# Performance work log

Hardware: AMD Instinct MI355X
Metric: run time of the kernel (lower is better)

## Reference

```python
import jax, jax.numpy as jnp
import numpy as np

L1_W = 0.5
L2_W = 0.5
THR_W = 0.5
NON_THR_W = 0.5


def setup_inputs() -> dict:
    key = jax.random.key(0)
    k1, k2 = jax.random.split(key)
    shape = (32, 3, 512, 512)
    input_img = jax.random.normal(k1, shape, dtype=jnp.float32)
    target_img = jax.random.normal(k2, shape, dtype=jnp.float32)
    return {"input_img": input_img, "target_img": target_img}


def _masked_mean(x, mask):
    # mean over elements where mask is True; 0.0 if mask is empty
    cnt = jnp.sum(mask)
    s = jnp.sum(jnp.where(mask, x, 0.0))
    return jnp.where(cnt > 0, s / jnp.maximum(cnt, 1).astype(x.dtype), jnp.zeros((), x.dtype))


def reference(input_img, target_img):
    diff = input_img - target_img
    pixel_diff = jnp.abs(diff)          # |x - y|
    pixel_diff_sq = diff * diff          # (x - y)^2

    mse_loss = jnp.mean(pixel_diff_sq)
    mae_loss = jnp.mean(pixel_diff)

    # adaptive thresholds (mse_threshold / mae_threshold were None)
    mse_thresholded_loss = _masked_mean(pixel_diff_sq, pixel_diff_sq >= mse_loss)
    mae_thresholded_loss = _masked_mean(pixel_diff, pixel_diff >= mae_loss)

    combined_thr = L1_W * mae_thresholded_loss + L2_W * mse_thresholded_loss
    combined_non_thr = L1_W * mae_loss + L2_W * mse_loss

    total_loss = THR_W * combined_thr + NON_THR_W * combined_non_thr
    return total_loss
```

## Files before the change

kernel.cpp:

```cpp
#include <hip/hip_runtime.h>


#define THREADS 256
#define NB 2048
#define UNROLL 4

__device__ __forceinline__ float wave_reduce_f(float v) {
    for (int o = 32; o > 0; o >>= 1) v += __shfl_down(v, o);
    return v;
}
__device__ __forceinline__ unsigned wave_reduce_u(unsigned v) {
    for (int o = 32; o > 0; o >>= 1) v += __shfl_down(v, o);
    return v;
}
__device__ __forceinline__ double wave_reduce_d(double v) {
    for (int o = 32; o > 0; o >>= 1) v += __shfl_down(v, o);
    return v;
}

__global__ void pass1_sums(const float4* __restrict__ a, const float4* __restrict__ b,
                           int n4, int n, float* __restrict__ psq, float* __restrict__ pab) {
    float ssq = 0.f, sab = 0.f;
    const int tile_total = gridDim.x * blockDim.x * UNROLL;
    const int n4_main = (n4 / tile_total) * tile_total;

    for (int base = (blockIdx.x * blockDim.x) * UNROLL + threadIdx.x;
         base < n4_main; base += tile_total) {
        float4 xa[UNROLL], xb[UNROLL];
#pragma unroll
        for (int j = 0; j < UNROLL; ++j) {
            xa[j] = a[base + j * THREADS];
            xb[j] = b[base + j * THREADS];
        }
#pragma unroll
        for (int j = 0; j < UNROLL; ++j) {
            float d0 = xa[j].x - xb[j].x, d1 = xa[j].y - xb[j].y;
            float d2 = xa[j].z - xb[j].z, d3 = xa[j].w - xb[j].w;
            ssq += d0 * d0 + d1 * d1 + d2 * d2 + d3 * d3;
            sab += fabsf(d0) + fabsf(d1) + fabsf(d2) + fabsf(d3);
        }
    }
    for (int i = n4_main + blockIdx.x * blockDim.x + threadIdx.x; i < n4;
         i += gridDim.x * blockDim.x) {
        float4 x = a[i], y = b[i];
        float d0 = x.x - y.x, d1 = x.y - y.y, d2 = x.z - y.z, d3 = x.w - y.w;
        ssq += d0 * d0 + d1 * d1 + d2 * d2 + d3 * d3;
        sab += fabsf(d0) + fabsf(d1) + fabsf(d2) + fabsf(d3);
    }
    const float* as = (const float*)a;
    const float* bs = (const float*)b;
    for (int i = n4 * 4 + blockIdx.x * blockDim.x + threadIdx.x; i < n;
         i += gridDim.x * blockDim.x) {
        float d = as[i] - bs[i];
        ssq += d * d;
        sab += fabsf(d);
    }

    ssq = wave_reduce_f(ssq);
    sab = wave_reduce_f(sab);
    __shared__ float s1[THREADS / 64], s2[THREADS / 64];
    int lane = threadIdx.x & 63, wave = threadIdx.x >> 6;
    if (lane == 0) { s1[wave] = ssq; s2[wave] = sab; }
    __syncthreads();
    if (threadIdx.x == 0) {
        float t1 = 0.f, t2 = 0.f;
        for (int w = 0; w < THREADS / 64; ++w) { t1 += s1[w]; t2 += s2[w]; }
        psq[blockIdx.x] = t1;
        pab[blockIdx.x] = t2;
    }
}

__global__ void finalize_means(const float* __restrict__ psq, const float* __restrict__ pab,
                               float* __restrict__ means, int nb, double inv_n) {
    double s1 = 0.0, s2 = 0.0;
    for (int i = threadIdx.x; i < nb; i += blockDim.x) { s1 += psq[i]; s2 += pab[i]; }
    s1 = wave_reduce_d(s1);
    s2 = wave_reduce_d(s2);
    __shared__ double w1[THREADS / 64], w2[THREADS / 64];
    int lane = threadIdx.x & 63, wave = threadIdx.x >> 6;
    if (lane == 0) { w1[wave] = s1; w2[wave] = s2; }
    __syncthreads();
    if (threadIdx.x == 0) {
        double t1 = 0.0, t2 = 0.0;
        for (int w = 0; w < THREADS / 64; ++w) { t1 += w1[w]; t2 += w2[w]; }
        means[0] = (float)(t1 * inv_n);
        means[1] = (float)(t2 * inv_n);
    }
}

__global__ void pass2_masked(const float4* __restrict__ a, const float4* __restrict__ b,
                             int n4, int n, const float* __restrict__ means,
                             float* __restrict__ p2sq, float* __restrict__ p2ab,
                             unsigned* __restrict__ p2c1, unsigned* __restrict__ p2c2) {
    const float mse = means[0];
    const float mae = means[1];
    float mssq = 0.f, msab = 0.f;
    unsigned c1 = 0, c2 = 0;
    const int tile_total = gridDim.x * blockDim.x * UNROLL;
    const int n4_main = (n4 / tile_total) * tile_total;

    for (int base = (blockIdx.x * blockDim.x) * UNROLL + threadIdx.x;
         base < n4_main; base += tile_total) {
        float4 xa[UNROLL], xb[UNROLL];
#pragma unroll
        for (int j = 0; j < UNROLL; ++j) {
            xa[j] = a[base + j * THREADS];
            xb[j] = b[base + j * THREADS];
        }
#pragma unroll
        for (int j = 0; j < UNROLL; ++j) {
            float d[4] = {xa[j].x - xb[j].x, xa[j].y - xb[j].y,
                          xa[j].z - xb[j].z, xa[j].w - xb[j].w};
#pragma unroll
            for (int k = 0; k < 4; ++k) {
                float dsq = d[k] * d[k];
                float ad = fabsf(d[k]);
                if (dsq >= mse) { mssq += dsq; c1++; }
                if (ad >= mae)  { msab += ad;  c2++; }
            }
        }
    }
    for (int i = n4_main + blockIdx.x * blockDim.x + threadIdx.x; i < n4;
         i += gridDim.x * blockDim.x) {
        float4 x = a[i], y = b[i];
        float d[4] = {x.x - y.x, x.y - y.y, x.z - y.z, x.w - y.w};
#pragma unroll
        for (int k = 0; k < 4; ++k) {
            float dsq = d[k] * d[k];
            float ad = fabsf(d[k]);
            if (dsq >= mse) { mssq += dsq; c1++; }
            if (ad >= mae)  { msab += ad;  c2++; }
        }
    }
    const float* as = (const float*)a;
    const float* bs = (const float*)b;
    for (int i = n4 * 4 + blockIdx.x * blockDim.x + threadIdx.x; i < n;
         i += gridDim.x * blockDim.x) {
        float d = as[i] - bs[i];
        float dsq = d * d;
        float ad = fabsf(d);
        if (dsq >= mse) { mssq += dsq; c1++; }
        if (ad >= mae)  { msab += ad;  c2++; }
    }

    mssq = wave_reduce_f(mssq);
    msab = wave_reduce_f(msab);
    c1 = wave_reduce_u(c1);
    c2 = wave_reduce_u(c2);
    __shared__ float s1[THREADS / 64], s2[THREADS / 64];
    __shared__ unsigned u1[THREADS / 64], u2[THREADS / 64];
    int lane = threadIdx.x & 63, wave = threadIdx.x >> 6;
    if (lane == 0) { s1[wave] = mssq; s2[wave] = msab; u1[wave] = c1; u2[wave] = c2; }
    __syncthreads();
    if (threadIdx.x == 0) {
        float t1 = 0.f, t2 = 0.f;
        unsigned k1 = 0, k2 = 0;
        for (int w = 0; w < THREADS / 64; ++w) { t1 += s1[w]; t2 += s2[w]; k1 += u1[w]; k2 += u2[w]; }
        p2sq[blockIdx.x] = t1;
        p2ab[blockIdx.x] = t2;
        p2c1[blockIdx.x] = k1;
        p2c2[blockIdx.x] = k2;
    }
}

__global__ void finalize_loss(const float* __restrict__ p2sq, const float* __restrict__ p2ab,
                              const unsigned* __restrict__ p2c1, const unsigned* __restrict__ p2c2,
                              const float* __restrict__ means, int nb, float* __restrict__ out) {
    double s1 = 0.0, s2 = 0.0;
    unsigned long long k1 = 0, k2 = 0;
    for (int i = threadIdx.x; i < nb; i += blockDim.x) {
        s1 += p2sq[i]; s2 += p2ab[i]; k1 += p2c1[i]; k2 += p2c2[i];
    }
    s1 = wave_reduce_d(s1);
    s2 = wave_reduce_d(s2);
    for (int o = 32; o > 0; o >>= 1) k1 += __shfl_down(k1, o);
    for (int o = 32; o > 0; o >>= 1) k2 += __shfl_down(k2, o);
    __shared__ double w1[THREADS / 64], w2[THREADS / 64];
    __shared__ unsigned long long v1[THREADS / 64], v2[THREADS / 64];
    int lane = threadIdx.x & 63, wave = threadIdx.x >> 6;
    if (lane == 0) { w1[wave] = s1; w2[wave] = s2; v1[wave] = k1; v2[wave] = k2; }
    __syncthreads();
    if (threadIdx.x == 0) {
        double t1 = 0.0, t2 = 0.0;
        unsigned long long c1 = 0, c2 = 0;
        for (int w = 0; w < THREADS / 64; ++w) { t1 += w1[w]; t2 += w2[w]; c1 += v1[w]; c2 += v2[w]; }
        double mse_thr = c1 ? t1 / (double)c1 : 0.0;
        double mae_thr = c2 ? t2 / (double)c2 : 0.0;
        double comb_thr = 0.5 * mae_thr + 0.5 * mse_thr;
        double comb_non = 0.5 * (double)means[1] + 0.5 * (double)means[0];
        out[0] = (float)(0.5 * comb_thr + 0.5 * comb_non);
    }
}

extern "C" void kernel_launch(void* const* d_in, const int* in_sizes, int n_in,
                              void* d_out, int out_size, void* d_ws, size_t ws_size,
                              hipStream_t stream) {
    const float* a = (const float*)d_in[0];
    const float* b = (const float*)d_in[1];
    const int n = in_sizes[0];
    const int n4 = n / 4;

    char* ws = (char*)d_ws;
    float* p1sq = (float*)(ws + 0);
    float* p1ab = (float*)(ws + 8192);
    float* p2sq = (float*)(ws + 16384);
    float* p2ab = (float*)(ws + 24576);
    unsigned* p2c1 = (unsigned*)(ws + 32768);
    unsigned* p2c2 = (unsigned*)(ws + 40960);
    float* means = (float*)(ws + 49152);

    pass1_sums<<<NB, THREADS, 0, stream>>>((const float4*)a, (const float4*)b, n4, n, p1sq, p1ab);
    finalize_means<<<1, THREADS, 0, stream>>>(p1sq, p1ab, means, NB, 1.0 / (double)n);
    pass2_masked<<<NB, THREADS, 0, stream>>>((const float4*)a, (const float4*)b, n4, n, means,
                                             p2sq, p2ab, p2c1, p2c2);
    finalize_loss<<<1, THREADS, 0, stream>>>(p2sq, p2ab, p2c1, p2c2, means, NB, (float*)d_out);
}
```

Baseline: 250.9 us.

## Fuse mean finalization into pass2 and specialize exact-size fully unrolled passes

Removes the separate finalize_means launch: every pass2 block re-reduces the 2048 pass1 partials itself to get the thresholds, and the final kernel recomputes the means. Adds a specialized path for the exact input size (32*3*512*512) where each thread handles 12 float4s with fixed indexing, batched loads, no tail loops, and branchless masked accumulation. The aim is to save one kernel launch and gap, and to get more memory-level parallelism per thread. In exchange, each pass2 block redundantly reads 16KB of partials, and the general fallback path is kept for other sizes.

```diff
diff --git a/kernel.cpp b/kernel.cpp
--- a/kernel.cpp
+++ b/kernel.cpp
@@ -3,7 +3,8 @@
 
 #define THREADS 256
 #define NB 2048
-#define UNROLL 4
+#define PER_THREAD 12
+#define BATCH 6
 
 __device__ __forceinline__ float wave_reduce_f(float v) {
     for (int o = 32; o > 0; o >>= 1) v += __shfl_down(v, o);
@@ -18,129 +19,112 @@
     return v;
 }
 
-__global__ void pass1_sums(const float4* __restrict__ a, const float4* __restrict__ b,
-                           int n4, int n, float* __restrict__ psq, float* __restrict__ pab) {
-    float ssq = 0.f, sab = 0.f;
-    const int tile_total = gridDim.x * blockDim.x * UNROLL;
-    const int n4_main = (n4 / tile_total) * tile_total;
-
-    for (int base = (blockIdx.x * blockDim.x) * UNROLL + threadIdx.x;
-         base < n4_main; base += tile_total) {
-        float4 xa[UNROLL], xb[UNROLL];
-#pragma unroll
-        for (int j = 0; j < UNROLL; ++j) {
-            xa[j] = a[base + j * THREADS];
-            xb[j] = b[base + j * THREADS];
-        }
-#pragma unroll
-        for (int j = 0; j < UNROLL; ++j) {
-            float d0 = xa[j].x - xb[j].x, d1 = xa[j].y - xb[j].y;
-            float d2 = xa[j].z - xb[j].z, d3 = xa[j].w - xb[j].w;
-            ssq += d0 * d0 + d1 * d1 + d2 * d2 + d3 * d3;
-            sab += fabsf(d0) + fabsf(d1) + fabsf(d2) + fabsf(d3);
-        }
-    }
-    for (int i = n4_main + blockIdx.x * blockDim.x + threadIdx.x; i < n4;
-         i += gridDim.x * blockDim.x) {
-        float4 x = a[i], y = b[i];
-        float d0 = x.x - y.x, d1 = x.y - y.y, d2 = x.z - y.z, d3 = x.w - y.w;
-        ssq += d0 * d0 + d1 * d1 + d2 * d2 + d3 * d3;
-        sab += fabsf(d0) + fabsf(d1) + fabsf(d2) + fabsf(d3);
-    }
-    const float* as = (const float*)a;
-    const float* bs = (const float*)b;
-    for (int i = n4 * 4 + blockIdx.x * blockDim.x + threadIdx.x; i < n;
-         i += gridDim.x * blockDim.x) {
-        float d = as[i] - bs[i];
-        ssq += d * d;
-        sab += fabsf(d);
-    }
-
-    ssq = wave_reduce_f(ssq);
-    sab = wave_reduce_f(sab);
+__device__ __forceinline__ void block_reduce_2f(float& v1, float& v2, float* out1, float* out2) {
+    v1 = wave_reduce_f(v1);
+    v2 = wave_reduce_f(v2);
     __shared__ float s1[THREADS / 64], s2[THREADS / 64];
     int lane = threadIdx.x & 63, wave = threadIdx.x >> 6;
-    if (lane == 0) { s1[wave] = ssq; s2[wave] = sab; }
+    if (lane == 0) { s1[wave] = v1; s2[wave] = v2; }
     __syncthreads();
     if (threadIdx.x == 0) {
         float t1 = 0.f, t2 = 0.f;
         for (int w = 0; w < THREADS / 64; ++w) { t1 += s1[w]; t2 += s2[w]; }
-        psq[blockIdx.x] = t1;
-        pab[blockIdx.x] = t2;
-    }
-}
-
-__global__ void finalize_means(const float* __restrict__ psq, const float* __restrict__ pab,
-                               float* __restrict__ means, int nb, double inv_n) {
+        out1[blockIdx.x] = t1;
+        out2[blockIdx.x] = t2;
+    }
+}
+
+__device__ __forceinline__ void compute_means(const float* __restrict__ p1sq,
+                                              const float* __restrict__ p1ab,
+                                              double inv_n, float& mse, float& mae) {
     double s1 = 0.0, s2 = 0.0;
-    for (int i = threadIdx.x; i < nb; i += blockDim.x) { s1 += psq[i]; s2 += pab[i]; }
+    for (int i = threadIdx.x; i < NB; i += THREADS) { s1 += p1sq[i]; s2 += p1ab[i]; }
     s1 = wave_reduce_d(s1);
     s2 = wave_reduce_d(s2);
     __shared__ double w1[THREADS / 64], w2[THREADS / 64];
+    __shared__ float bm[2];
     int lane = threadIdx.x & 63, wave = threadIdx.x >> 6;
     if (lane == 0) { w1[wave] = s1; w2[wave] = s2; }
     __syncthreads();
     if (threadIdx.x == 0) {
         double t1 = 0.0, t2 = 0.0;
         for (int w = 0; w < THREADS / 64; ++w) { t1 += w1[w]; t2 += w2[w]; }
-        means[0] = (float)(t1 * inv_n);
-        means[1] = (float)(t2 * inv_n);
-    }
-}
-
-__global__ void pass2_masked(const float4* __restrict__ a, const float4* __restrict__ b,
-                             int n4, int n, const float* __restrict__ means,
-                             float* __restrict__ p2sq, float* __restrict__ p2ab,
-                             unsigned* __restrict__ p2c1, unsigned* __restrict__ p2c2) {
-    const float mse = means[0];
-    const float mae = means[1];
+        bm[0] = (float)(t1 * inv_n);
+        bm[1] = (float)(t2 * inv_n);
+    }
+    __syncthreads();
+    mse = bm[0];
+    mae = bm[1];
+    __syncthreads();
+}
+
+
+__global__ __launch_bounds__(THREADS) void pass1_s(const float4* __restrict__ a,
+                                                   const float4* __restrict__ b,
+                                                   float* __restrict__ psq,
+                                                   float* __restrict__ pab) {
+    const int i0 = blockIdx.x * (THREADS * PER_THREAD) + threadIdx.x;
+    float s0 = 0.f, s1 = 0.f, a0 = 0.f, a1 = 0.f;
+#pragma unroll
+    for (int h = 0; h < PER_THREAD / BATCH; ++h) {
+        const int base = i0 + h * BATCH * THREADS;
+        float4 xa[BATCH], xb[BATCH];
+#pragma unroll
+        for (int j = 0; j < BATCH; ++j) xa[j] = a[base + j * THREADS];
+#pragma unroll
+        for (int j = 0; j < BATCH; ++j) xb[j] = b[base + j * THREADS];
+#pragma unroll
+        for (int j = 0; j < BATCH; ++j) {
+            float d0 = xa[j].x - xb[j].x, d1 = xa[j].y - xb[j].y;
+            float d2 = xa[j].z - xb[j].z, d3 = xa[j].w - xb[j].w;
+            s0 += d0 * d0 + d1 * d1;
+            s1 += d2 * d2 + d3 * d3;
+            a0 += fabsf(d0) + fabsf(d1);
+            a1 += fabsf(d2) + fabsf(d3);
+        }
+    }
+    float ssq = s0 + s1, sab = a0 + a1;
+    block_reduce_2f(ssq, sab, psq, pab);
+}
+
+__global__ __launch_bounds__(THREADS) void pass2_s(const float4* __restrict__ a,
+                                                   const float4* __restrict__ b,
+                                                   const float* __restrict__ p1sq,
+                                                   const float* __restrict__ p1ab,
+                                                   double inv_n,
+                                                   float* __restrict__ p2sq,
+                                                   float* __restrict__ p2ab,
+                                                   unsigned* __restrict__ p2c1,
+                                                   unsigned* __restrict__ p2c2) {
+    float mse, mae;
+    compute_means(p1sq, p1ab, inv_n, mse, mae);
+
+    const int i0 = blockIdx.x * (THREADS * PER_THREAD) + threadIdx.x;
     float mssq = 0.f, msab = 0.f;
     unsigned c1 = 0, c2 = 0;
-    const int tile_total = gridDim.x * blockDim.x * UNROLL;
-    const int n4_main = (n4 / tile_total) * tile_total;
-
-    for (int base = (blockIdx.x * blockDim.x) * UNROLL + threadIdx.x;
-         base < n4_main; base += tile_total) {
-        float4 xa[UNROLL], xb[UNROLL];
-#pragma unroll
-        for (int j = 0; j < UNROLL; ++j) {
-            xa[j] = a[base + j * THREADS];
-            xb[j] = b[base + j * THREADS];
-        }
-#pragma unroll
-        for (int j = 0; j < UNROLL; ++j) {
+#pragma unroll
+    for (int h = 0; h < PER_THREAD / BATCH; ++h) {
+        const int base = i0 + h * BATCH * THREADS;
+        float4 xa[BATCH], xb[BATCH];
+#pragma unroll
+        for (int j = 0; j < BATCH; ++j) xa[j] = a[base + j * THREADS];
+#pragma unroll
+        for (int j = 0; j < BATCH; ++j) xb[j] = b[base + j * THREADS];
+#pragma unroll
+        for (int j = 0; j < BATCH; ++j) {
             float d[4] = {xa[j].x - xb[j].x, xa[j].y - xb[j].y,
                           xa[j].z - xb[j].z, xa[j].w - xb[j].w};
 #pragma unroll
             for (int k = 0; k < 4; ++k) {
                 float dsq = d[k] * d[k];
                 float ad = fabsf(d[k]);
-                if (dsq >= mse) { mssq += dsq; c1++; }
-                if (ad >= mae)  { msab += ad;  c2++; }
+                bool m1 = dsq >= mse, m2 = ad >= mae;
+                mssq += m1 ? dsq : 0.f;
+                msab += m2 ? ad : 0.f;
+                c1 += m1 ? 1u : 0u;
+                c2 += m2 ? 1u : 0u;
             }
         }
-    }
-    for (int i = n4_main + blockIdx.x * blockDim.x + threadIdx.x; i < n4;
-         i += gridDim.x * blockDim.x) {
-        float4 x = a[i], y = b[i];
-        float d[4] = {x.x - y.x, x.y - y.y, x.z - y.z, x.w - y.w};
-#pragma unroll
-        for (int k = 0; k < 4; ++k) {
-            float dsq = d[k] * d[k];
-            float ad = fabsf(d[k]);
-            if (dsq >= mse) { mssq += dsq; c1++; }
-            if (ad >= mae)  { msab += ad;  c2++; }
-        }
-    }
-    const float* as = (const float*)a;
-    const float* bs = (const float*)b;
-    for (int i = n4 * 4 + blockIdx.x * blockDim.x + threadIdx.x; i < n;
-         i += gridDim.x * blockDim.x) {
-        float d = as[i] - bs[i];
-        float dsq = d * d;
-        float ad = fabsf(d);
-        if (dsq >= mse) { mssq += dsq; c1++; }
-        if (ad >= mae)  { msab += ad;  c2++; }
     }
 
     mssq = wave_reduce_f(mssq);
@@ -163,32 +147,110 @@
     }
 }
 
-__global__ void finalize_loss(const float* __restrict__ p2sq, const float* __restrict__ p2ab,
-                              const unsigned* __restrict__ p2c1, const unsigned* __restrict__ p2c2,
-                              const float* __restrict__ means, int nb, float* __restrict__ out) {
-    double s1 = 0.0, s2 = 0.0;
+__global__ void finalize_loss_s(const float* __restrict__ p1sq, const float* __restrict__ p1ab,
+                                const float* __restrict__ p2sq, const float* __restrict__ p2ab,
+                                const unsigned* __restrict__ p2c1, const unsigned* __restrict__ p2c2,
+                                double inv_n, float* __restrict__ out) {
+    double s1 = 0.0, s2 = 0.0, m1 = 0.0, m2 = 0.0;
     unsigned long long k1 = 0, k2 = 0;
-    for (int i = threadIdx.x; i < nb; i += blockDim.x) {
-        s1 += p2sq[i]; s2 += p2ab[i]; k1 += p2c1[i]; k2 += p2c2[i];
-    }
-    s1 = wave_reduce_d(s1);
-    s2 = wave_reduce_d(s2);
+    for (int i = threadIdx.x; i < NB; i += blockDim.x) {
+        m1 += p1sq[i]; m2 += p1ab[i];
+        s1 += p2sq[i]; s2 += p2ab[i];
+        k1 += p2c1[i]; k2 += p2c2[i];
+    }
+    s1 = wave_reduce_d(s1); s2 = wave_reduce_d(s2);
+    m1 = wave_reduce_d(m1); m2 = wave_reduce_d(m2);
     for (int o = 32; o > 0; o >>= 1) k1 += __shfl_down(k1, o);
     for (int o = 32; o > 0; o >>= 1) k2 += __shfl_down(k2, o);
-    __shared__ double w1[THREADS / 64], w2[THREADS / 64];
+    __shared__ double w1[THREADS / 64], w2[THREADS / 64], w3[THREADS / 64], w4[THREADS / 64];
     __shared__ unsigned long long v1[THREADS / 64], v2[THREADS / 64];
     int lane = threadIdx.x & 63, wave = threadIdx.x >> 6;
-    if (lane == 0) { w1[wave] = s1; w2[wave] = s2; v1[wave] = k1; v2[wave] = k2; }
-    __syncthreads();
-    if (threadIdx.x == 0) {
-        double t1 = 0.0, t2 = 0.0;
+    if (lane == 0) { w1[wave] = s1; w2[wave] = s2; w3[wave] = m1; w4[wave] = m2; v1[wave] = k1; v2[wave] = k2; }
+    __syncthreads();
+    if (threadIdx.x == 0) {
+        double t1 = 0.0, t2 = 0.0, q1 = 0.0, q2 = 0.0;
         unsigned long long c1 = 0, c2 = 0;
-        for (int w = 0; w < THREADS / 64; ++w) { t1 += w1[w]; t2 += w2[w]; c1 += v1[w]; c2 += v2[w]; }
+        for (int w = 0; w < THREADS / 64; ++w) {
+            t1 += w1[w]; t2 += w2[w]; q1 += w3[w]; q2 += w4[w]; c1 += v1[w]; c2 += v2[w];
+        }
+        float mse = (float)(q1 * inv_n);
+        float mae = (float)(q2 * inv_n);
         double mse_thr = c1 ? t1 / (double)c1 : 0.0;
         double mae_thr = c2 ? t2 / (double)c2 : 0.0;
         double comb_thr = 0.5 * mae_thr + 0.5 * mse_thr;
-        double comb_non = 0.5 * (double)means[1] + 0.5 * (double)means[0];
+        double comb_non = 0.5 * (double)mae + 0.5 * (double)mse;
         out[0] = (float)(0.5 * comb_thr + 0.5 * comb_non);
+    }
+}
+
+
+__global__ void pass1_g(const float4* __restrict__ a, const float4* __restrict__ b,
+                        int n4, int n, float* __restrict__ psq, float* __restrict__ pab) {
+    float ssq = 0.f, sab = 0.f;
+    const int stride = gridDim.x * blockDim.x;
+    for (int i = blockIdx.x * blockDim.x + threadIdx.x; i < n4; i += stride) {
+        float4 x = a[i], y = b[i];
+        float d0 = x.x - y.x, d1 = x.y - y.y, d2 = x.z - y.z, d3 = x.w - y.w;
+        ssq += d0 * d0 + d1 * d1 + d2 * d2 + d3 * d3;
+        sab += fabsf(d0) + fabsf(d1) + fabsf(d2) + fabsf(d3);
+    }
+    const float* as = (const float*)a;
+    const float* bs = (const float*)b;
+    for (int i = n4 * 4 + blockIdx.x * blockDim.x + threadIdx.x; i < n; i += stride) {
+        float d = as[i] - bs[i];
+        ssq += d * d;
+        sab += fabsf(d);
+    }
+    block_reduce_2f(ssq, sab, psq, pab);
+}
+
+__global__ void pass2_g(const float4* __restrict__ a, const float4* __restrict__ b,
+                        int n4, int n, const float* __restrict__ p1sq,
+                        const float* __restrict__ p1ab, double inv_n,
+                        float* __restrict__ p2sq, float* __restrict__ p2ab,
+                        unsigned* __restrict__ p2c1, unsigned* __restrict__ p2c2) {
+    float mse, mae;
+    compute_means(p1sq, p1ab, inv_n, mse, mae);
+    float mssq = 0.f, msab = 0.f;
+    unsigned c1 = 0, c2 = 0;
+    const int stride = gridDim.x * blockDim.x;
+    for (int i = blockIdx.x * blockDim.x + threadIdx.x; i < n4; i += stride) {
+        float4 x = a[i], y = b[i];
+        float d[4] = {x.x - y.x, x.y - y.y, x.z - y.z, x.w - y.w};
+#pragma unroll
+        for (int k = 0; k < 4; ++k) {
+            float dsq = d[k] * d[k];
+            float ad = fabsf(d[k]);
+            if (dsq >= mse) { mssq += dsq; c1++; }
+            if (ad >= mae)  { msab += ad;  c2++; }
+        }
+    }
+    const float* as = (const float*)a;
+    const float* bs = (const float*)b;
+    for (int i = n4 * 4 + blockIdx.x * blockDim.x + threadIdx.x; i < n; i += stride) {
+        float d = as[i] - bs[i];
+        float dsq = d * d;
+        float ad = fabsf(d);
+        if (dsq >= mse) { mssq += dsq; c1++; }
+        if (ad >= mae)  { msab += ad;  c2++; }
+    }
+    mssq = wave_reduce_f(mssq);
+    msab = wave_reduce_f(msab);
+    c1 = wave_reduce_u(c1);
+    c2 = wave_reduce_u(c2);
+    __shared__ float s1[THREADS / 64], s2[THREADS / 64];
+    __shared__ unsigned u1[THREADS / 64], u2[THREADS / 64];
+    int lane = threadIdx.x & 63, wave = threadIdx.x >> 6;
+    if (lane == 0) { s1[wave] = mssq; s2[wave] = msab; u1[wave] = c1; u2[wave] = c2; }
+    __syncthreads();
+    if (threadIdx.x == 0) {
+        float t1 = 0.f, t2 = 0.f;
+        unsigned k1 = 0, k2 = 0;
+        for (int w = 0; w < THREADS / 64; ++w) { t1 += s1[w]; t2 += s2[w]; k1 += u1[w]; k2 += u2[w]; }
+        p2sq[blockIdx.x] = t1;
+        p2ab[blockIdx.x] = t2;
+        p2c1[blockIdx.x] = k1;
+        p2c2[blockIdx.x] = k2;
     }
 }
 
@@ -207,11 +269,18 @@
     float* p2ab = (float*)(ws + 24576);
     unsigned* p2c1 = (unsigned*)(ws + 32768);
     unsigned* p2c2 = (unsigned*)(ws + 40960);
-    float* means = (float*)(ws + 49152);
-
-    pass1_sums<<<NB, THREADS, 0, stream>>>((const float4*)a, (const float4*)b, n4, n, p1sq, p1ab);
-    finalize_means<<<1, THREADS, 0, stream>>>(p1sq, p1ab, means, NB, 1.0 / (double)n);
-    pass2_masked<<<NB, THREADS, 0, stream>>>((const float4*)a, (const float4*)b, n4, n, means,
-                                             p2sq, p2ab, p2c1, p2c2);
-    finalize_loss<<<1, THREADS, 0, stream>>>(p2sq, p2ab, p2c1, p2c2, means, NB, (float*)d_out);
-}
+
+    const double inv_n = 1.0 / (double)n;
+
+    if (n4 == NB * THREADS * PER_THREAD && n % 4 == 0) {
+        pass1_s<<<NB, THREADS, 0, stream>>>((const float4*)a, (const float4*)b, p1sq, p1ab);
+        pass2_s<<<NB, THREADS, 0, stream>>>((const float4*)a, (const float4*)b, p1sq, p1ab,
+                                            inv_n, p2sq, p2ab, p2c1, p2c2);
+    } else {
+        pass1_g<<<NB, THREADS, 0, stream>>>((const float4*)a, (const float4*)b, n4, n, p1sq, p1ab);
+        pass2_g<<<NB, THREADS, 0, stream>>>((const float4*)a, (const float4*)b, n4, n,
+                                            p1sq, p1ab, inv_n, p2sq, p2ab, p2c1, p2c2);
+    }
+    finalize_loss_s<<<1, THREADS, 0, stream>>>(p1sq, p1ab, p2sq, p2ab, p2c1, p2c2,
+                                               inv_n, (float*)d_out);
+}
```

Result: no change. 251.5 us (+0.2%).
